# Optimization experiments

Measured on AMD Instinct MI355X. Metric: run time of the kernel, lower is better.

Reference implementation:

```python
import jax, jax.numpy as jnp
import numpy as np

B, T, C = 2, 2048, 1024
H, D = 16, 64


def setup_inputs() -> dict:
    key = jax.random.key(0)
    ks = jax.random.split(key, 5)
    s = 1.0 / np.sqrt(C)  # keep projections well-scaled
    return {
        "x": jax.random.normal(ks[0], (B, T, C), dtype=jnp.float32),
        "wq": jax.random.normal(ks[1], (C, C), dtype=jnp.float32) * s,
        "wk": jax.random.normal(ks[2], (C, C), dtype=jnp.float32) * s,
        "wv": jax.random.normal(ks[3], (C, C), dtype=jnp.float32) * s,
        "wo": jax.random.normal(ks[4], (C, C), dtype=jnp.float32) * s,
    }


def reference(x, wq, wk, wv, wo):
    # nn.Linear(d,d,bias=False): y = x @ W.T ; weights stored [out,in]
    q = (x @ wq.T).reshape(B, T, H, D).transpose(0, 2, 1, 3)  # [B,H,T,D]
    k = (x @ wk.T).reshape(B, T, H, D).transpose(0, 2, 1, 3)
    v = (x @ wv.T).reshape(B, T, H, D).transpose(0, 2, 1, 3)
    scale = jnp.sqrt(jnp.float32(D))
    scores = jnp.einsum("bhtd,bhsd->bhts", q, k) / scale  # [B,H,T,T]
    # additive causal mask: -inf above the diagonal
    causal = jnp.tril(jnp.ones((T, T), dtype=bool))
    scores = jnp.where(causal[None, None], scores, jnp.float32(-1e9))
    weights = jax.nn.softmax(scores, axis=-1)
    out = jnp.einsum("bhts,bhsd->bhtd", weights, v)  # [B,H,T,D]
    out = out.transpose(0, 2, 1, 3).reshape(B, T, C)
    return out @ wo.T
```

## Files before the change

kernel.cpp:

```cpp
#include <hip/hip_runtime.h>
#include <stdint.h>

#define B_ 2
#define T_ 2048
#define C_ 1024
#define H_ 16
#define D_ 64
#define M_ (B_*T_)

typedef __attribute__((ext_vector_type(8))) short bf16x8;
typedef __attribute__((ext_vector_type(4))) short bf16x4;
typedef __attribute__((ext_vector_type(4))) float f32x4;
typedef unsigned short u16;

#define MFMA32(a, b, c) __builtin_amdgcn_mfma_f32_16x16x32_bf16((a), (b), (c), 0, 0, 0)

__device__ __forceinline__ u16 f2bf(float f) {
  union { float f; uint32_t u; } v; v.f = f;
  uint32_t u = v.u;
  return (u16)((u + 0x7fffu + ((u >> 16) & 1u)) >> 16);
}

__device__ __forceinline__ float exp2_fast(float x) { return __builtin_amdgcn_exp2f(x); }

typedef const __attribute__((address_space(1))) void* gas_t;
typedef __attribute__((address_space(3))) void* las_t;
__device__ __forceinline__ void gld_lds16(const void* g, void* l) {
  __builtin_amdgcn_global_load_lds((gas_t)g, (las_t)l, 16, 0, 0);
}

__global__ void cvt_all(const float* __restrict__ x,
                        const float* __restrict__ w0, const float* __restrict__ w1,
                        const float* __restrict__ w2, const float* __restrict__ w3,
                        u16* __restrict__ xb,
                        u16* __restrict__ d0, u16* __restrict__ d1,
                        u16* __restrict__ d2, u16* __restrict__ d3) {
  size_t i = ((size_t)blockIdx.x * 256 + threadIdx.x) * 4;
  const float* s; u16* d; size_t off;
  const size_t NX = (size_t)M_ * C_;
  const size_t NW = (size_t)C_ * C_;
  if (i < NX) { s = x; d = xb; off = i; }
  else {
    size_t j = i - NX;
    int w = (int)(j / NW); off = j - (size_t)w * NW;
    switch (w) {
      case 0: s = w0; d = d0; break;
      case 1: s = w1; d = d1; break;
      case 2: s = w2; d = d2; break;
      default: s = w3; d = d3; break;
    }
  }
  float4 v = *(const float4*)(s + off);
  ushort4 o;
  o.x = f2bf(v.x); o.y = f2bf(v.y); o.z = f2bf(v.z); o.w = f2bf(v.w);
  *(ushort4*)(d + off) = o;
}

__device__ __forceinline__ void gemm_core(const u16* __restrict__ A,
                                          const u16* __restrict__ W,
                                          int m0, int n0, int Kt,
                                          f32x4 acc[4][4])
{
  __shared__ u16 As[128*64];
  __shared__ u16 Bs[128*64];
  const int t = threadIdx.x;
  const int lane = t & 63;
  const int wave = t >> 6;
  const int q = lane >> 4;
  const int l15 = lane & 15;
  const int wm = (wave >> 1) * 64;
  const int wn = (wave & 1) * 64;

  #pragma unroll
  for (int i = 0; i < 4; ++i)
    #pragma unroll
    for (int j = 0; j < 4; ++j)
      acc[i][j] = (f32x4){0.f, 0.f, 0.f, 0.f};

  for (int k0 = 0; k0 < Kt; k0 += 64) {
    #pragma unroll
    for (int r = 0; r < 4; ++r) {
      int Lc = r * 256 + t;
      int row = Lc >> 3;
      int gcc = (Lc & 7) ^ (row & 7);
      gld_lds16(A + (size_t)(m0 + row) * Kt + k0 + gcc * 8, As + Lc * 8);
    }
    #pragma unroll
    for (int r = 0; r < 4; ++r) {
      int Lc = r * 256 + t;
      int row = Lc >> 3;
      int gcc = (Lc & 7) ^ (row & 7);
      gld_lds16(W + (size_t)(n0 + row) * Kt + k0 + gcc * 8, Bs + Lc * 8);
    }
    __syncthreads();

    #pragma unroll
    for (int kk = 0; kk < 2; ++kk) {
      bf16x8 af[4], bfr[4];
      #pragma unroll
      for (int i = 0; i < 4; ++i) {
        int m = wm + i * 16 + l15;
        int ch = (kk * 4 + q) ^ (m & 7);
        af[i] = *(const bf16x8*)(As + m * 64 + ch * 8);
      }
      #pragma unroll
      for (int j = 0; j < 4; ++j) {
        int n = wn + j * 16 + l15;
        int ch = (kk * 4 + q) ^ (n & 7);
        bfr[j] = *(const bf16x8*)(Bs + n * 64 + ch * 8);
      }
      #pragma unroll
      for (int i = 0; i < 4; ++i)
        #pragma unroll
        for (int j = 0; j < 4; ++j)
          acc[i][j] = MFMA32(af[i], bfr[j], acc[i][j]);
    }
    __syncthreads();
  }
}

#define QSCALE 0.1803368801111244f
__global__ __launch_bounds__(256, 3)
void gemm_qkv(const u16* __restrict__ X,
              const u16* __restrict__ Wq, const u16* __restrict__ Wk,
              const u16* __restrict__ Wv,
              u16* __restrict__ Q, u16* __restrict__ K, u16* __restrict__ Vt)
{
  const int bm = blockIdx.x;
  const int bn = blockIdx.y;
  const int seg = bn >> 3;
  const int nb = (bn & 7) * 128;

  const int t = threadIdx.x, lane = t & 63, wave = t >> 6;
  const int q = lane >> 4, l15 = lane & 15;
  const int wm = (wave >> 1) * 64, wn = (wave & 1) * 64;

  f32x4 acc[4][4];

  if (seg < 2) {
    const u16* W = (seg == 0) ? Wq : Wk;
    gemm_core(W, X, nb, bm * 128, C_, acc);
    u16* dst = (seg == 0) ? Q : K;
    const float scale = (seg == 0) ? QSCALE : 1.0f;
    #pragma unroll
    for (int i = 0; i < 4; ++i) {
      #pragma unroll
      for (int j = 0; j < 4; ++j) {
        const int o = nb + wm + i * 16 + q * 4;
        const int h = o >> 6, d = o & 63;
        const int mtok = bm * 128 + wn + j * 16 + l15;
        const int b = mtok >> 11, tt = mtok & (T_ - 1);
        ushort4 pk;
        pk.x = f2bf(acc[i][j][0] * scale); pk.y = f2bf(acc[i][j][1] * scale);
        pk.z = f2bf(acc[i][j][2] * scale); pk.w = f2bf(acc[i][j][3] * scale);
        *(ushort4*)(dst + (((size_t)(b * H_ + h)) * T_ + tt) * D_ + d) = pk;
      }
    }
  } else {
    gemm_core(X, Wv, bm * 128, nb, C_, acc);
    #pragma unroll
    for (int i = 0; i < 4; ++i) {
      #pragma unroll
      for (int j = 0; j < 4; ++j) {
        const int mbase = bm * 128 + wm + i * 16 + q * 4;
        const int b = mbase >> 11, tt = mbase & (T_ - 1);
        const int n = nb + wn + j * 16 + l15;
        const int h = n >> 6, d = n & 63;
        const int ttp = (tt & ~31) | ((tt & 12) << 1) | ((tt & 16) >> 2);
        size_t idx = (((size_t)(b * H_ + h)) * D_ + d) * T_ + ttp;
        ushort4 pk;
        pk.x = f2bf(acc[i][j][0]); pk.y = f2bf(acc[i][j][1]);
        pk.z = f2bf(acc[i][j][2]); pk.w = f2bf(acc[i][j][3]);
        *(ushort4*)(Vt + idx) = pk;
      }
    }
  }
}

__global__ __launch_bounds__(256, 2)
void attn(const u16* __restrict__ Q, const u16* __restrict__ K,
          const u16* __restrict__ Vt, u16* __restrict__ Att)
{
  __shared__ u16 Ks[2][128 * 64];
  __shared__ u16 Vs[2][64 * 128];
  const int t = threadIdx.x;
  const int lane = t & 63, wave = t >> 6;
  const int q = lane >> 4, l15 = lane & 15;
  const int pr = blockIdx.x;
  const int bh = blockIdx.y;
  const int qbA = pr * 64;
  const int qbB = (31 - pr) * 64;
  const u16* Qp = Q + (size_t)bh * T_ * D_;
  const u16* Kp = K + (size_t)bh * T_ * D_;
  const u16* Vp = Vt + (size_t)bh * D_ * T_;

  const int rowA = qbA + 4 * l15 + wave;
  const int rowB = qbB + 4 * l15 + wave;
  const u16* qra = Qp + (size_t)rowA * 64;
  const u16* qrb = Qp + (size_t)rowB * 64;
  const bf16x8 aqA0 = *(const bf16x8*)(qra + q * 8);
  const bf16x8 aqA1 = *(const bf16x8*)(qra + 32 + q * 8);
  const bf16x8 aqB0 = *(const bf16x8*)(qrb + q * 8);
  const bf16x8 aqB1 = *(const bf16x8*)(qrb + 32 + q * 8);

  f32x4 oA[4], oB[4];
  #pragma unroll
  for (int j = 0; j < 4; ++j) {
    oA[j] = (f32x4){0.f, 0.f, 0.f, 0.f};
    oB[j] = (f32x4){0.f, 0.f, 0.f, 0.f};
  }
  float lsA = 0.f, lsB = 0.f;

  auto stage = [&](int kb, int buf) {
    #pragma unroll
    for (int r = 0; r < 4; ++r) {
      int c = r * 256 + t, row = c >> 3, gcc = (c & 7) ^ (row & 7);
      gld_lds16(Kp + (size_t)(kb + row) * 64 + gcc * 8, &Ks[buf][c * 8]);
    }
    #pragma unroll
    for (int r = 0; r < 4; ++r) {
      int c = r * 256 + t, row = c >> 4, gcc = (c & 15) ^ (row & 15);
      gld_lds16(Vp + (size_t)row * T_ + kb + gcc * 8, &Vs[buf][c * 8]);
    }
  };

  stage(0, 0);
  int cur = 0;
  for (int kb = 0; kb <= qbB; kb += 128, cur ^= 1) {
    __syncthreads();
    if (kb + 128 <= qbB) stage(kb + 128, cur ^ 1);
    const u16* Kc = &Ks[cur][0];
    const u16* Vc = &Vs[cur][0];

    #pragma unroll
    for (int s = 0; s < 2; ++s) {
      const int kbase = kb + s * 64;
      if (kbase > qbB) break;

      bf16x8 kf0[4], kf1[4];
      #pragma unroll
      for (int j2 = 0; j2 < 4; ++j2) {
        const int rw = s * 64 + j2 * 16 + l15;
        kf0[j2] = *(const bf16x8*)(Kc + rw * 64 + ((q)     ^ (rw & 7)) * 8);
        kf1[j2] = *(const bf16x8*)(Kc + rw * 64 + ((4 + q) ^ (rw & 7)) * 8);
      }
      bf16x8 vfrag[4][2];
      #pragma unroll
      for (int j = 0; j < 4; ++j) {
        const int rw = j * 16 + l15;
        #pragma unroll
        for (int kk = 0; kk < 2; ++kk) {
          const int cc = ((2 * s + kk) * 4 + q) ^ (rw & 15);
          vfrag[j][kk] = *(const bf16x8*)(Vc + rw * 128 + cc * 8);
        }
      }

      auto tile_compute = [&](const bf16x8 a0, const bf16x8 a1, f32x4* o,
                              float& lsum, int rowg, bool diag) {
        bf16x4 pb[4];
        #pragma unroll
        for (int j2 = 0; j2 < 4; ++j2) {
          f32x4 z = (f32x4){0.f, 0.f, 0.f, 0.f};
          z = MFMA32(kf0[j2], a0, z);
          z = MFMA32(kf1[j2], a1, z);
          if (diag) {
            #pragma unroll
            for (int r = 0; r < 4; ++r) {
              const int key = kbase + j2 * 16 + q * 4 + r;
              if (key > rowg) z[r] = -1e30f;
            }
          }
          float p0 = exp2_fast(z[0]), p1 = exp2_fast(z[1]);
          float p2 = exp2_fast(z[2]), p3 = exp2_fast(z[3]);
          lsum += (p0 + p1) + (p2 + p3);
          pb[j2] = (bf16x4){(short)f2bf(p0), (short)f2bf(p1),
                            (short)f2bf(p2), (short)f2bf(p3)};
        }
        #pragma unroll
        for (int kk = 0; kk < 2; ++kk) {
          const bf16x8 pc = __builtin_shufflevector(pb[2 * kk], pb[2 * kk + 1],
                                                    0, 1, 2, 3, 4, 5, 6, 7);
          #pragma unroll
          for (int j = 0; j < 4; ++j)
            o[j] = MFMA32(vfrag[j][kk], pc, o[j]);
        }
      };

      tile_compute(aqB0, aqB1, oB, lsB, rowB, kbase == qbB);
      if (kbase <= qbA)
        tile_compute(aqA0, aqA1, oA, lsA, rowA, kbase == qbA);
    }
  }

  lsA += __shfl_xor(lsA, 16, 64); lsA += __shfl_xor(lsA, 32, 64);
  lsB += __shfl_xor(lsB, 16, 64); lsB += __shfl_xor(lsB, 32, 64);
  const float invA = __builtin_amdgcn_rcpf(lsA);
  const float invB = __builtin_amdgcn_rcpf(lsB);

  const int b = bh >> 4, h = bh & 15;
  #pragma unroll
  for (int j = 0; j < 4; ++j) {
    ushort4 pa, pbk;
    pa.x = f2bf(oA[j][0] * invA); pa.y = f2bf(oA[j][1] * invA);
    pa.z = f2bf(oA[j][2] * invA); pa.w = f2bf(oA[j][3] * invA);
    pbk.x = f2bf(oB[j][0] * invB); pbk.y = f2bf(oB[j][1] * invB);
    pbk.z = f2bf(oB[j][2] * invB); pbk.w = f2bf(oB[j][3] * invB);
    *(ushort4*)(Att + ((size_t)b * T_ + rowA) * C_ + h * 64 + j * 16 + q * 4) = pa;
    *(ushort4*)(Att + ((size_t)b * T_ + rowB) * C_ + h * 64 + j * 16 + q * 4) = pbk;
  }
}

__global__ __launch_bounds__(256, 2)
void gemm_out(const u16* __restrict__ Att, const u16* __restrict__ Wo,
              float* __restrict__ Out)
{
  __shared__ u16 As[64 * 64];
  __shared__ u16 Bs[128 * 64];
  const int t = threadIdx.x;
  const int lane = t & 63, wave = t >> 6;
  const int q = lane >> 4, l15 = lane & 15;
  const int wm = (wave >> 1) * 32, wn = (wave & 1) * 64;
  const int m0 = blockIdx.x * 64;
  const int n0 = blockIdx.y * 128;

  f32x4 acc[2][4];
  #pragma unroll
  for (int i = 0; i < 2; ++i)
    #pragma unroll
    for (int j = 0; j < 4; ++j)
      acc[i][j] = (f32x4){0.f, 0.f, 0.f, 0.f};

  for (int k0 = 0; k0 < C_; k0 += 64) {
    #pragma unroll
    for (int r = 0; r < 2; ++r) {
      int Lc = r * 256 + t, row = Lc >> 3, gcc = (Lc & 7) ^ (row & 7);
      gld_lds16(Wo + (size_t)(m0 + row) * C_ + k0 + gcc * 8, As + Lc * 8);
    }
    #pragma unroll
    for (int r = 0; r < 4; ++r) {
      int Lc = r * 256 + t, row = Lc >> 3, gcc = (Lc & 7) ^ (row & 7);
      gld_lds16(Att + (size_t)(n0 + row) * C_ + k0 + gcc * 8, Bs + Lc * 8);
    }
    __syncthreads();

    #pragma unroll
    for (int kk = 0; kk < 2; ++kk) {
      bf16x8 af[2], bfr[4];
      #pragma unroll
      for (int i = 0; i < 2; ++i) {
        int m = wm + i * 16 + l15;
        int ch = (kk * 4 + q) ^ (m & 7);
        af[i] = *(const bf16x8*)(As + m * 64 + ch * 8);
      }
      #pragma unroll
      for (int j = 0; j < 4; ++j) {
        int n = wn + j * 16 + l15;
        int ch = (kk * 4 + q) ^ (n & 7);
        bfr[j] = *(const bf16x8*)(Bs + n * 64 + ch * 8);
      }
      #pragma unroll
      for (int i = 0; i < 2; ++i)
        #pragma unroll
        for (int j = 0; j < 4; ++j)
          acc[i][j] = MFMA32(af[i], bfr[j], acc[i][j]);
    }
    __syncthreads();
  }

  #pragma unroll
  for (int i = 0; i < 2; ++i) {
    #pragma unroll
    for (int j = 0; j < 4; ++j) {
      const int o = m0 + wm + i * 16 + q * 4;
      const int tok = n0 + wn + j * 16 + l15;
      float4 st = {acc[i][j][0], acc[i][j][1], acc[i][j][2], acc[i][j][3]};
      *(float4*)(Out + (size_t)tok * C_ + o) = st;
    }
  }
}

extern "C" void kernel_launch(void* const* d_in, const int* in_sizes, int n_in,
                              void* d_out, int out_size, void* d_ws, size_t ws_size,
                              hipStream_t stream) {
  const float* x  = (const float*)d_in[0];
  const float* wq = (const float*)d_in[1];
  const float* wk = (const float*)d_in[2];
  const float* wv = (const float*)d_in[3];
  const float* wo = (const float*)d_in[4];
  float* out = (float*)d_out;

  u16* ws  = (u16*)d_ws;
  u16* xb  = ws;
  u16* wqb = xb  + (size_t)M_ * C_;
  u16* wkb = wqb + (size_t)C_ * C_;
  u16* wvb = wkb + (size_t)C_ * C_;
  u16* wob = wvb + (size_t)C_ * C_;
  u16* Qb  = wob + (size_t)C_ * C_;
  u16* Kb  = Qb  + (size_t)M_ * C_;
  u16* Vtb = Kb  + (size_t)M_ * C_;
  u16* Atb = Vtb + (size_t)M_ * C_;

  cvt_all<<<dim3((M_ * C_ + 4 * C_ * C_) / 1024), 256, 0, stream>>>(
      x, wq, wk, wv, wo, xb, wqb, wkb, wvb, wob);

  gemm_qkv<<<dim3(M_ / 128, 24), 256, 0, stream>>>(xb, wqb, wkb, wvb, Qb, Kb, Vtb);
  attn<<<dim3(16, B_ * H_), 256, 0, stream>>>(Qb, Kb, Vtb, Atb);
  gemm_out<<<dim3(C_ / 64, M_ / 128), 256, 0, stream>>>(Atb, wob, out);
}
```

Measured before the change: 171.1 us.

## Split attention key range across two blocks, merge partials in output GEMM

Each attention block now handles only even or odd 64-key tiles, doubling the grid to 32x32 blocks with smaller LDS tiles and a higher occupancy bound. Unnormalized partial outputs and row sums are written to two buffers, and the output projection GEMM sums the partials, normalizes, and writes bf16 into LDS through register loads instead of direct global-to-LDS loads. The goal is more parallelism and better load balance in attention, at the cost of extra partial-buffer traffic and a heavier B-operand load in gemm_out. Merging without a max rescale works because the scores are never max-subtracted, which already held before.

```diff
diff --git a/kernel.cpp b/kernel.cpp
--- a/kernel.cpp
+++ b/kernel.cpp
@@ -19,6 +19,12 @@
   union { float f; uint32_t u; } v; v.f = f;
   uint32_t u = v.u;
   return (u16)((u + 0x7fffu + ((u >> 16) & 1u)) >> 16);
+}
+__device__ __forceinline__ float bf2f_lo(uint32_t u) {
+  union { uint32_t u; float f; } v; v.u = u << 16; return v.f;
+}
+__device__ __forceinline__ float bf2f_hi(uint32_t u) {
+  union { uint32_t u; float f; } v; v.u = u & 0xffff0000u; return v.f;
 }
 
 __device__ __forceinline__ float exp2_fast(float x) { return __builtin_amdgcn_exp2f(x); }
@@ -177,16 +183,19 @@
   }
 }
 
-__global__ __launch_bounds__(256, 2)
+__global__ __launch_bounds__(256, 4)
 void attn(const u16* __restrict__ Q, const u16* __restrict__ K,
-          const u16* __restrict__ Vt, u16* __restrict__ Att)
+          const u16* __restrict__ Vt,
+          u16* __restrict__ O0, u16* __restrict__ O1,
+          float* __restrict__ L0, float* __restrict__ L1)
 {
-  __shared__ u16 Ks[2][128 * 64];
-  __shared__ u16 Vs[2][64 * 128];
+  __shared__ u16 Ks[2][64 * 64];
+  __shared__ u16 Vs[2][64 * 64];
   const int t = threadIdx.x;
   const int lane = t & 63, wave = t >> 6;
   const int q = lane >> 4, l15 = lane & 15;
-  const int pr = blockIdx.x;
+  const int pr = blockIdx.x >> 1;
+  const int hf = blockIdx.x & 1;
   const int bh = blockIdx.y;
   const int qbA = pr * 64;
   const int qbB = (31 - pr) * 64;
@@ -213,106 +222,106 @@
 
   auto stage = [&](int kb, int buf) {
     #pragma unroll
-    for (int r = 0; r < 4; ++r) {
-      int c = r * 256 + t, row = c >> 3, gcc = (c & 7) ^ (row & 7);
-      gld_lds16(Kp + (size_t)(kb + row) * 64 + gcc * 8, &Ks[buf][c * 8]);
-    }
-    #pragma unroll
-    for (int r = 0; r < 4; ++r) {
-      int c = r * 256 + t, row = c >> 4, gcc = (c & 15) ^ (row & 15);
-      gld_lds16(Vp + (size_t)row * T_ + kb + gcc * 8, &Vs[buf][c * 8]);
+    for (int r = 0; r < 2; ++r) {
+      int c = r * 256 + t, rw = c >> 3, gcc = (c & 7) ^ (rw & 7);
+      gld_lds16(Kp + (size_t)(kb + rw) * 64 + gcc * 8, &Ks[buf][c * 8]);
+    }
+    #pragma unroll
+    for (int r = 0; r < 2; ++r) {
+      int c = r * 256 + t, rw = c >> 3, gcc = (c & 7) ^ (rw & 7);
+      gld_lds16(Vp + (size_t)rw * T_ + kb + gcc * 8, &Vs[buf][c * 8]);
     }
   };
 
-  stage(0, 0);
+  const int kb0 = hf * 64;
+  stage(kb0, 0);
   int cur = 0;
-  for (int kb = 0; kb <= qbB; kb += 128, cur ^= 1) {
+  for (int kb = kb0; kb <= qbB; kb += 128, cur ^= 1) {
     __syncthreads();
     if (kb + 128 <= qbB) stage(kb + 128, cur ^ 1);
     const u16* Kc = &Ks[cur][0];
     const u16* Vc = &Vs[cur][0];
 
-    #pragma unroll
-    for (int s = 0; s < 2; ++s) {
-      const int kbase = kb + s * 64;
-      if (kbase > qbB) break;
-
-      bf16x8 kf0[4], kf1[4];
+    bf16x8 kf0[4], kf1[4];
+    #pragma unroll
+    for (int j2 = 0; j2 < 4; ++j2) {
+      const int rw = j2 * 16 + l15;
+      kf0[j2] = *(const bf16x8*)(Kc + rw * 64 + ((q)     ^ (rw & 7)) * 8);
+      kf1[j2] = *(const bf16x8*)(Kc + rw * 64 + ((4 + q) ^ (rw & 7)) * 8);
+    }
+    bf16x8 vfrag[4][2];
+    #pragma unroll
+    for (int j = 0; j < 4; ++j) {
+      const int rw = j * 16 + l15;
+      #pragma unroll
+      for (int kk = 0; kk < 2; ++kk) {
+        const int ch = (kk * 4 + q) ^ (rw & 7);
+        vfrag[j][kk] = *(const bf16x8*)(Vc + rw * 64 + ch * 8);
+      }
+    }
+
+    auto tile_compute = [&](const bf16x8 a0, const bf16x8 a1, f32x4* o,
+                            float& lsum, int rowg, bool diag) {
+      bf16x4 pb[4];
       #pragma unroll
       for (int j2 = 0; j2 < 4; ++j2) {
-        const int rw = s * 64 + j2 * 16 + l15;
-        kf0[j2] = *(const bf16x8*)(Kc + rw * 64 + ((q)     ^ (rw & 7)) * 8);
-        kf1[j2] = *(const bf16x8*)(Kc + rw * 64 + ((4 + q) ^ (rw & 7)) * 8);
-      }
-      bf16x8 vfrag[4][2];
-      #pragma unroll
-      for (int j = 0; j < 4; ++j) {
-        const int rw = j * 16 + l15;
+        f32x4 z = (f32x4){0.f, 0.f, 0.f, 0.f};
+        z = MFMA32(kf0[j2], a0, z);
+        z = MFMA32(kf1[j2], a1, z);
+        if (diag) {
+          #pragma unroll
+          for (int r = 0; r < 4; ++r) {
+            const int key = kb + j2 * 16 + q * 4 + r;
+            if (key > rowg) z[r] = -1e30f;
+          }
+        }
+        float p0 = exp2_fast(z[0]), p1 = exp2_fast(z[1]);
+        float p2 = exp2_fast(z[2]), p3 = exp2_fast(z[3]);
+        lsum += (p0 + p1) + (p2 + p3);
+        pb[j2] = (bf16x4){(short)f2bf(p0), (short)f2bf(p1),
+                          (short)f2bf(p2), (short)f2bf(p3)};
+      }
+      #pragma unroll
+      for (int kk = 0; kk < 2; ++kk) {
+        const bf16x8 pc = __builtin_shufflevector(pb[2 * kk], pb[2 * kk + 1],
+                                                  0, 1, 2, 3, 4, 5, 6, 7);
         #pragma unroll
-        for (int kk = 0; kk < 2; ++kk) {
-          const int cc = ((2 * s + kk) * 4 + q) ^ (rw & 15);
-          vfrag[j][kk] = *(const bf16x8*)(Vc + rw * 128 + cc * 8);
-        }
-      }
-
-      auto tile_compute = [&](const bf16x8 a0, const bf16x8 a1, f32x4* o,
-                              float& lsum, int rowg, bool diag) {
-        bf16x4 pb[4];
-        #pragma unroll
-        for (int j2 = 0; j2 < 4; ++j2) {
-          f32x4 z = (f32x4){0.f, 0.f, 0.f, 0.f};
-          z = MFMA32(kf0[j2], a0, z);
-          z = MFMA32(kf1[j2], a1, z);
-          if (diag) {
-            #pragma unroll
-            for (int r = 0; r < 4; ++r) {
-              const int key = kbase + j2 * 16 + q * 4 + r;
-              if (key > rowg) z[r] = -1e30f;
-            }
-          }
-          float p0 = exp2_fast(z[0]), p1 = exp2_fast(z[1]);
-          float p2 = exp2_fast(z[2]), p3 = exp2_fast(z[3]);
-          lsum += (p0 + p1) + (p2 + p3);
-          pb[j2] = (bf16x4){(short)f2bf(p0), (short)f2bf(p1),
-                            (short)f2bf(p2), (short)f2bf(p3)};
-        }
-        #pragma unroll
-        for (int kk = 0; kk < 2; ++kk) {
-          const bf16x8 pc = __builtin_shufflevector(pb[2 * kk], pb[2 * kk + 1],
-                                                    0, 1, 2, 3, 4, 5, 6, 7);
-          #pragma unroll
-          for (int j = 0; j < 4; ++j)
-            o[j] = MFMA32(vfrag[j][kk], pc, o[j]);
-        }
-      };
-
-      tile_compute(aqB0, aqB1, oB, lsB, rowB, kbase == qbB);
-      if (kbase <= qbA)
-        tile_compute(aqA0, aqA1, oA, lsA, rowA, kbase == qbA);
-    }
+        for (int j = 0; j < 4; ++j)
+          o[j] = MFMA32(vfrag[j][kk], pc, o[j]);
+      }
+    };
+
+    tile_compute(aqB0, aqB1, oB, lsB, rowB, kb == qbB);
+    if (kb <= qbA)
+      tile_compute(aqA0, aqA1, oA, lsA, rowA, kb == qbA);
   }
 
   lsA += __shfl_xor(lsA, 16, 64); lsA += __shfl_xor(lsA, 32, 64);
   lsB += __shfl_xor(lsB, 16, 64); lsB += __shfl_xor(lsB, 32, 64);
-  const float invA = __builtin_amdgcn_rcpf(lsA);
-  const float invB = __builtin_amdgcn_rcpf(lsB);
-
+
+  u16* Oh = hf ? O1 : O0;
+  float* Lh = hf ? L1 : L0;
+  if (q == 0) {
+    Lh[(size_t)bh * T_ + rowA] = lsA;
+    Lh[(size_t)bh * T_ + rowB] = lsB;
+  }
   const int b = bh >> 4, h = bh & 15;
   #pragma unroll
   for (int j = 0; j < 4; ++j) {
     ushort4 pa, pbk;
-    pa.x = f2bf(oA[j][0] * invA); pa.y = f2bf(oA[j][1] * invA);
-    pa.z = f2bf(oA[j][2] * invA); pa.w = f2bf(oA[j][3] * invA);
-    pbk.x = f2bf(oB[j][0] * invB); pbk.y = f2bf(oB[j][1] * invB);
-    pbk.z = f2bf(oB[j][2] * invB); pbk.w = f2bf(oB[j][3] * invB);
-    *(ushort4*)(Att + ((size_t)b * T_ + rowA) * C_ + h * 64 + j * 16 + q * 4) = pa;
-    *(ushort4*)(Att + ((size_t)b * T_ + rowB) * C_ + h * 64 + j * 16 + q * 4) = pbk;
+    pa.x = f2bf(oA[j][0]); pa.y = f2bf(oA[j][1]);
+    pa.z = f2bf(oA[j][2]); pa.w = f2bf(oA[j][3]);
+    pbk.x = f2bf(oB[j][0]); pbk.y = f2bf(oB[j][1]);
+    pbk.z = f2bf(oB[j][2]); pbk.w = f2bf(oB[j][3]);
+    *(ushort4*)(Oh + ((size_t)b * T_ + rowA) * C_ + h * 64 + j * 16 + q * 4) = pa;
+    *(ushort4*)(Oh + ((size_t)b * T_ + rowB) * C_ + h * 64 + j * 16 + q * 4) = pbk;
   }
 }
 
 __global__ __launch_bounds__(256, 2)
-void gemm_out(const u16* __restrict__ Att, const u16* __restrict__ Wo,
-              float* __restrict__ Out)
+void gemm_out(const u16* __restrict__ O0, const u16* __restrict__ O1,
+              const float* __restrict__ L0, const float* __restrict__ L1,
+              const u16* __restrict__ Wo, float* __restrict__ Out)
 {
   __shared__ u16 As[64 * 64];
   __shared__ u16 Bs[128 * 64];
@@ -336,10 +345,29 @@
       int Lc = r * 256 + t, row = Lc >> 3, gcc = (Lc & 7) ^ (row & 7);
       gld_lds16(Wo + (size_t)(m0 + row) * C_ + k0 + gcc * 8, As + Lc * 8);
     }
+    const int head = k0 >> 6;
     #pragma unroll
     for (int r = 0; r < 4; ++r) {
       int Lc = r * 256 + t, row = Lc >> 3, gcc = (Lc & 7) ^ (row & 7);
-      gld_lds16(Att + (size_t)(n0 + row) * C_ + k0 + gcc * 8, Bs + Lc * 8);
+      const int tok = n0 + row;
+      const int bhl = (tok >> 11) * H_ + head;
+      const int tloc = tok & (T_ - 1);
+      const float inv = __builtin_amdgcn_rcpf(
+          L0[(size_t)bhl * T_ + tloc] + L1[(size_t)bhl * T_ + tloc]);
+      const size_t src = (size_t)tok * C_ + k0 + gcc * 8;
+      uint4 a = *(const uint4*)(O0 + src);
+      uint4 bb = *(const uint4*)(O1 + src);
+      ushort4 w0, w1;
+      w0.x = f2bf((bf2f_lo(a.x) + bf2f_lo(bb.x)) * inv);
+      w0.y = f2bf((bf2f_hi(a.x) + bf2f_hi(bb.x)) * inv);
+      w0.z = f2bf((bf2f_lo(a.y) + bf2f_lo(bb.y)) * inv);
+      w0.w = f2bf((bf2f_hi(a.y) + bf2f_hi(bb.y)) * inv);
+      w1.x = f2bf((bf2f_lo(a.z) + bf2f_lo(bb.z)) * inv);
+      w1.y = f2bf((bf2f_hi(a.z) + bf2f_hi(bb.z)) * inv);
+      w1.z = f2bf((bf2f_lo(a.w) + bf2f_lo(bb.w)) * inv);
+      w1.w = f2bf((bf2f_hi(a.w) + bf2f_hi(bb.w)) * inv);
+      *(ushort4*)(Bs + Lc * 8)     = w0;
+      *(ushort4*)(Bs + Lc * 8 + 4) = w1;
     }
     __syncthreads();
 
@@ -398,12 +426,15 @@
   u16* Qb  = wob + (size_t)C_ * C_;
   u16* Kb  = Qb  + (size_t)M_ * C_;
   u16* Vtb = Kb  + (size_t)M_ * C_;
-  u16* Atb = Vtb + (size_t)M_ * C_;
+  u16* O0b = Vtb + (size_t)M_ * C_;
+  u16* O1b = O0b + (size_t)M_ * C_;
+  float* L0b = (float*)(O1b + (size_t)M_ * C_);
+  float* L1b = L0b + (size_t)(B_ * H_) * T_;
 
   cvt_all<<<dim3((M_ * C_ + 4 * C_ * C_) / 1024), 256, 0, stream>>>(
       x, wq, wk, wv, wo, xb, wqb, wkb, wvb, wob);
 
   gemm_qkv<<<dim3(M_ / 128, 24), 256, 0, stream>>>(xb, wqb, wkb, wvb, Qb, Kb, Vtb);
-  attn<<<dim3(16, B_ * H_), 256, 0, stream>>>(Qb, Kb, Vtb, Atb);
-  gemm_out<<<dim3(C_ / 64, M_ / 128), 256, 0, stream>>>(Atb, wob, out);
-}
+  attn<<<dim3(32, B_ * H_), 256, 0, stream>>>(Qb, Kb, Vtb, O0b, O1b, L0b, L1b);
+  gemm_out<<<dim3(C_ / 64, M_ / 128), 256, 0, stream>>>(O0b, O1b, L0b, L1b, wob, out);
+}
```

Result: slower. 239.2 us (+39.8%).

## Split attention key tiles across two wave groups with LDS reduction

Applied to the files above, without the earlier changes.

Doubles the attention block to 512 threads, so each 128-key tile is split into two 64-key halves processed by separate groups of four waves instead of one wave looping over both. Partial output accumulators and row sums from the second half are passed through shared memory as bf16 and combined by the first half before normalisation. Probabilities are now converted to bf16 by truncation rather than round-to-nearest, to save instructions. This adds parallelism per block and occupancy at the cost of an extra reduction step, two barriers, and small precision loss from truncation and the bf16 partial exchange.

```diff
diff --git a/kernel.cpp b/kernel.cpp
--- a/kernel.cpp
+++ b/kernel.cpp
@@ -19,6 +19,13 @@
   union { float f; uint32_t u; } v; v.f = f;
   uint32_t u = v.u;
   return (u16)((u + 0x7fffu + ((u >> 16) & 1u)) >> 16);
+}
+__device__ __forceinline__ u16 f2bf_t(float f) {
+  union { float f; uint32_t u; } v; v.f = f;
+  return (u16)(v.u >> 16);
+}
+__device__ __forceinline__ float bf2f(u16 u) {
+  union { uint32_t u; float f; } v; v.u = (uint32_t)u << 16; return v.f;
 }
 
 __device__ __forceinline__ float exp2_fast(float x) { return __builtin_amdgcn_exp2f(x); }
@@ -177,7 +184,7 @@
   }
 }
 
-__global__ __launch_bounds__(256, 2)
+__global__ __launch_bounds__(512, 4)
 void attn(const u16* __restrict__ Q, const u16* __restrict__ K,
           const u16* __restrict__ Vt, u16* __restrict__ Att)
 {
@@ -185,6 +192,7 @@
   __shared__ u16 Vs[2][64 * 128];
   const int t = threadIdx.x;
   const int lane = t & 63, wave = t >> 6;
+  const int w4 = wave & 3, half = wave >> 2;
   const int q = lane >> 4, l15 = lane & 15;
   const int pr = blockIdx.x;
   const int bh = blockIdx.y;
@@ -194,8 +202,8 @@
   const u16* Kp = K + (size_t)bh * T_ * D_;
   const u16* Vp = Vt + (size_t)bh * D_ * T_;
 
-  const int rowA = qbA + 4 * l15 + wave;
-  const int rowB = qbB + 4 * l15 + wave;
+  const int rowA = qbA + 4 * l15 + w4;
+  const int rowB = qbB + 4 * l15 + w4;
   const u16* qra = Qp + (size_t)rowA * 64;
   const u16* qrb = Qp + (size_t)rowB * 64;
   const bf16x8 aqA0 = *(const bf16x8*)(qra + q * 8);
@@ -213,13 +221,13 @@
 
   auto stage = [&](int kb, int buf) {
     #pragma unroll
-    for (int r = 0; r < 4; ++r) {
-      int c = r * 256 + t, row = c >> 3, gcc = (c & 7) ^ (row & 7);
+    for (int r = 0; r < 2; ++r) {
+      int c = r * 512 + t, row = c >> 3, gcc = (c & 7) ^ (row & 7);
       gld_lds16(Kp + (size_t)(kb + row) * 64 + gcc * 8, &Ks[buf][c * 8]);
     }
     #pragma unroll
-    for (int r = 0; r < 4; ++r) {
-      int c = r * 256 + t, row = c >> 4, gcc = (c & 15) ^ (row & 15);
+    for (int r = 0; r < 2; ++r) {
+      int c = r * 512 + t, row = c >> 4, gcc = (c & 15) ^ (row & 15);
       gld_lds16(Vp + (size_t)row * T_ + kb + gcc * 8, &Vs[buf][c * 8]);
     }
   };
@@ -232,15 +240,12 @@
     const u16* Kc = &Ks[cur][0];
     const u16* Vc = &Vs[cur][0];
 
-    #pragma unroll
-    for (int s = 0; s < 2; ++s) {
-      const int kbase = kb + s * 64;
-      if (kbase > qbB) break;
-
+    const int kbase = kb + half * 64;
+    if (kbase <= qbB) {
       bf16x8 kf0[4], kf1[4];
       #pragma unroll
       for (int j2 = 0; j2 < 4; ++j2) {
-        const int rw = s * 64 + j2 * 16 + l15;
+        const int rw = half * 64 + j2 * 16 + l15;
         kf0[j2] = *(const bf16x8*)(Kc + rw * 64 + ((q)     ^ (rw & 7)) * 8);
         kf1[j2] = *(const bf16x8*)(Kc + rw * 64 + ((4 + q) ^ (rw & 7)) * 8);
       }
@@ -250,7 +255,7 @@
         const int rw = j * 16 + l15;
         #pragma unroll
         for (int kk = 0; kk < 2; ++kk) {
-          const int cc = ((2 * s + kk) * 4 + q) ^ (rw & 15);
+          const int cc = ((2 * half + kk) * 4 + q) ^ (rw & 15);
           vfrag[j][kk] = *(const bf16x8*)(Vc + rw * 128 + cc * 8);
         }
       }
@@ -273,8 +278,8 @@
           float p0 = exp2_fast(z[0]), p1 = exp2_fast(z[1]);
           float p2 = exp2_fast(z[2]), p3 = exp2_fast(z[3]);
           lsum += (p0 + p1) + (p2 + p3);
-          pb[j2] = (bf16x4){(short)f2bf(p0), (short)f2bf(p1),
-                            (short)f2bf(p2), (short)f2bf(p3)};
+          pb[j2] = (bf16x4){(short)f2bf_t(p0), (short)f2bf_t(p1),
+                            (short)f2bf_t(p2), (short)f2bf_t(p3)};
         }
         #pragma unroll
         for (int kk = 0; kk < 2; ++kk) {
@@ -294,19 +299,49 @@
 
   lsA += __shfl_xor(lsA, 16, 64); lsA += __shfl_xor(lsA, 32, 64);
   lsB += __shfl_xor(lsB, 16, 64); lsB += __shfl_xor(lsB, 32, 64);
-  const float invA = __builtin_amdgcn_rcpf(lsA);
-  const float invB = __builtin_amdgcn_rcpf(lsB);
-
-  const int b = bh >> 4, h = bh & 15;
-  #pragma unroll
-  for (int j = 0; j < 4; ++j) {
-    ushort4 pa, pbk;
-    pa.x = f2bf(oA[j][0] * invA); pa.y = f2bf(oA[j][1] * invA);
-    pa.z = f2bf(oA[j][2] * invA); pa.w = f2bf(oA[j][3] * invA);
-    pbk.x = f2bf(oB[j][0] * invB); pbk.y = f2bf(oB[j][1] * invB);
-    pbk.z = f2bf(oB[j][2] * invB); pbk.w = f2bf(oB[j][3] * invB);
-    *(ushort4*)(Att + ((size_t)b * T_ + rowA) * C_ + h * 64 + j * 16 + q * 4) = pa;
-    *(ushort4*)(Att + ((size_t)b * T_ + rowB) * C_ + h * 64 + j * 16 + q * 4) = pbk;
+
+  u16* mo = &Ks[0][0];
+  float* ml = (float*)&Vs[0][0];
+  __syncthreads();
+  if (half == 1) {
+    const int base = (w4 * 64 + lane) * 32;
+    #pragma unroll
+    for (int j = 0; j < 4; ++j) {
+      ushort4 pa, pbk;
+      pa.x = f2bf(oA[j][0]); pa.y = f2bf(oA[j][1]);
+      pa.z = f2bf(oA[j][2]); pa.w = f2bf(oA[j][3]);
+      pbk.x = f2bf(oB[j][0]); pbk.y = f2bf(oB[j][1]);
+      pbk.z = f2bf(oB[j][2]); pbk.w = f2bf(oB[j][3]);
+      *(ushort4*)(mo + base + j * 4)      = pa;
+      *(ushort4*)(mo + base + 16 + j * 4) = pbk;
+    }
+    ml[(w4 * 64 + lane) * 2]     = lsA;
+    ml[(w4 * 64 + lane) * 2 + 1] = lsB;
+  }
+  __syncthreads();
+  if (half == 0) {
+    const int base = (w4 * 64 + lane) * 32;
+    lsA += ml[(w4 * 64 + lane) * 2];
+    lsB += ml[(w4 * 64 + lane) * 2 + 1];
+    const float invA = __builtin_amdgcn_rcpf(lsA);
+    const float invB = __builtin_amdgcn_rcpf(lsB);
+    const int b = bh >> 4, h = bh & 15;
+    #pragma unroll
+    for (int j = 0; j < 4; ++j) {
+      ushort4 ma = *(const ushort4*)(mo + base + j * 4);
+      ushort4 mb = *(const ushort4*)(mo + base + 16 + j * 4);
+      ushort4 pa, pbk;
+      pa.x = f2bf((oA[j][0] + bf2f(ma.x)) * invA);
+      pa.y = f2bf((oA[j][1] + bf2f(ma.y)) * invA);
+      pa.z = f2bf((oA[j][2] + bf2f(ma.z)) * invA);
+      pa.w = f2bf((oA[j][3] + bf2f(ma.w)) * invA);
+      pbk.x = f2bf((oB[j][0] + bf2f(mb.x)) * invB);
+      pbk.y = f2bf((oB[j][1] + bf2f(mb.y)) * invB);
+      pbk.z = f2bf((oB[j][2] + bf2f(mb.z)) * invB);
+      pbk.w = f2bf((oB[j][3] + bf2f(mb.w)) * invB);
+      *(ushort4*)(Att + ((size_t)b * T_ + rowA) * C_ + h * 64 + j * 16 + q * 4) = pa;
+      *(ushort4*)(Att + ((size_t)b * T_ + rowB) * C_ + h * 64 + j * 16 + q * 4) = pbk;
+    }
   }
 }
 
@@ -404,6 +439,6 @@
       x, wq, wk, wv, wo, xb, wqb, wkb, wvb, wob);
 
   gemm_qkv<<<dim3(M_ / 128, 24), 256, 0, stream>>>(xb, wqb, wkb, wvb, Qb, Kb, Vtb);
-  attn<<<dim3(16, B_ * H_), 256, 0, stream>>>(Qb, Kb, Vtb, Atb);
+  attn<<<dim3(16, B_ * H_), 512, 0, stream>>>(Qb, Kb, Vtb, Atb);
   gemm_out<<<dim3(C_ / 64, M_ / 128), 256, 0, stream>>>(Atb, wob, out);
 }
```

New measurement: 211.2 us. 1.23x slower.
